# Kernel optimization log

Hardware: AMD Instinct MI355X
Metric: run time of the kernel (lower is better)

## Reference

```python
import jax, jax.numpy as jnp
import numpy as np

N = 4096   # total atoms in batch
G = 32     # graphs in batch
T = 4      # number of atom types


def setup_inputs() -> dict:
    key = jax.random.key(0)
    ks = jax.random.split(key, 12)
    types = jax.random.randint(ks[0], (N,), 0, T)
    node_attrs = jax.nn.one_hot(types, T, dtype=jnp.float32)
    batch = jnp.repeat(jnp.arange(G, dtype=jnp.int32), N // G)  # sorted graph ids
    # interatomic distances, kept away from 0 to avoid 1/R**6 blowup
    R = jax.random.uniform(ks[1], (N, N), minval=0.5, maxval=5.0, dtype=jnp.float32)
    R = 0.5 * (R + R.T)
    F_cut = jax.random.uniform(ks[2], (N, N), dtype=jnp.float32)
    ref_A = jax.random.uniform(ks[3], (T, T), dtype=jnp.float32)
    ref_B = jax.random.uniform(ks[4], (T, T), dtype=jnp.float32)
    ref_C = jax.random.uniform(ks[5], (T, T), dtype=jnp.float32)
    ref_D = jax.random.uniform(ks[6], (T, T), dtype=jnp.float32)
    ref_mu = jax.random.uniform(ks[7], (T, T), dtype=jnp.float32)
    electric_energy = jax.random.normal(ks[8], (G, 1), dtype=jnp.float32)
    atomic_electric_energy = jax.random.normal(ks[9], (N, 1), dtype=jnp.float32)
    short_energy = jax.random.normal(ks[10], (G, 1), dtype=jnp.float32)
    atomic_short_energy = jax.random.normal(ks[11], (N, 1), dtype=jnp.float32)
    return dict(node_attrs=node_attrs, R=R, F_cut=F_cut,
                ref_A=ref_A, ref_B=ref_B, ref_C=ref_C, ref_D=ref_D, ref_mu=ref_mu,
                electric_energy=electric_energy,
                atomic_electric_energy=atomic_electric_energy,
                short_energy=short_energy, atomic_short_energy=atomic_short_energy,
                batch=batch)


def reference(node_attrs, R, F_cut, ref_A, ref_B, ref_C, ref_D, ref_mu,
              electric_energy, atomic_electric_energy,
              short_energy, atomic_short_energy, batch):
    n = node_attrs.shape[0]
    types = jnp.argmax(node_attrs, axis=1)                 # [N] atom type ids
    ti, tj = types[:, None], types[None, :]
    # intra-graph (block-diagonal) mask replaces the per-graph Python loop
    same = (batch[:, None] == batch[None, :]).astype(R.dtype)  # [N,N]
    A = ref_A[ti, tj]
    B = ref_B[ti, tj]
    C = ref_C[ti, tj]
    D = ref_D[ti, tj]
    mu = ref_mu[ti, tj]
    R6 = R ** 6
    # Buckingham-like pair potential; zero off-block and on the diagonal
    E_2b_ij = (A * jnp.exp(B * (mu - R)) - C / R6 - D / (R6 * R * R)) * F_cut * same
    E_2b_ij = jnp.where(jnp.eye(n, dtype=bool), jnp.zeros((), E_2b_ij.dtype), E_2b_ij)
    atomic_E_2b = (jnp.sum(E_2b_ij, axis=-1) * 0.5)[:, None]   # [N,1]
    E_2b = jax.ops.segment_sum(atomic_E_2b, batch, num_segments=G)  # [G,1]
    energy = electric_energy + E_2b + short_energy                   # [G,1]
    node_energy = atomic_electric_energy + atomic_E_2b + atomic_short_energy  # [N,1]
    return energy, node_energy
```

## Files before the change

kernel.cpp:

```cpp
#include <hip/hip_runtime.h>


template <int GSZ, int BPG>
__global__ __launch_bounds__(256) void te_part_kernel(
    const float* __restrict__ node_attrs,
    const float* __restrict__ Rm,
    const float* __restrict__ Fm,
    const float* __restrict__ rA,
    const float* __restrict__ rB,
    const float* __restrict__ rC,
    const float* __restrict__ rD,
    const float* __restrict__ rMu,
    const float* __restrict__ aelec,
    const float* __restrict__ ashort,
    const int* __restrict__ batch,
    float* __restrict__ out,
    float* __restrict__ ws,
    int n, int g) {
  constexpr int RPB = GSZ / BPG;
  constexpr int WAVES = 4;
  constexpr int RPW = RPB / WAVES;
  constexpr int CPL = GSZ / 64;

  const int b = blockIdx.x / BPG;
  const int c = blockIdx.x % BPG;
  const int gbase = b * GSZ;

  __shared__ float tab[5 * 16];
  __shared__ int   stype[GSZ];
  __shared__ int   sbatch[GSZ];
  __shared__ float wpart[WAVES];

  const int t = threadIdx.x;
  const int wave = t >> 6;
  const int lane = t & 63;
  const int row0 = c * RPB + wave * RPW;

  float rv[RPW][CPL], fv[RPW][CPL];
#pragma unroll
  for (int r = 0; r < RPW; ++r) {
    const size_t off = (size_t)(gbase + row0 + r) * n + gbase;
#pragma unroll
    for (int q = 0; q < CPL; ++q) {
      rv[r][q] = Rm[off + lane + q * 64];
      fv[r][q] = Fm[off + lane + q * 64];
    }
  }

  if (t < 16) {
    tab[t]      = rA[t];
    tab[16 + t] = rB[t];
    tab[32 + t] = rC[t];
    tab[48 + t] = rD[t];
    tab[64 + t] = rMu[t];
  }
  if (t < GSZ) {
    const float4 v = *(const float4*)(node_attrs + (size_t)(gbase + t) * 4);
    int bt = 0;
    float best = v.x;
    if (v.y > best) { best = v.y; bt = 1; }
    if (v.z > best) { best = v.z; bt = 2; }
    if (v.w > best) { best = v.w; bt = 3; }
    stype[t]  = bt;
    sbatch[t] = batch[gbase + t];
  }
  __syncthreads();

  float bpart = 0.f;
#pragma unroll
  for (int r = 0; r < RPW; ++r) {
    const int rl  = row0 + r;
    const int bi  = sbatch[rl];
    const int ti4 = stype[rl] * 4;
    float acc = 0.f;
#pragma unroll
    for (int q = 0; q < CPL; ++q) {
      const int jl = lane + q * 64;
      if (sbatch[jl] == bi && jl != rl) {
        float rr = rv[r][q];
        float f  = fv[r][q];
        int idx = ti4 + stype[jl];
        float r2 = rr * rr;
        float r6 = r2 * r2 * r2;
        float val = tab[idx] * __expf(tab[16 + idx] * (tab[64 + idx] - rr))
                    - tab[32 + idx] / r6
                    - tab[48 + idx] / (r6 * r2);
        acc += val * f;
      }
    }
#pragma unroll
    for (int o = 32; o > 0; o >>= 1) acc += __shfl_down(acc, o, 64);
    if (lane == 0) {
      const int gi = gbase + rl;
      float half = 0.5f * acc;
      out[g + gi] = aelec[gi] + half + ashort[gi];
      bpart += half;
    }
  }
  if (lane == 0) wpart[wave] = bpart;
  __syncthreads();

  if (t == 0) {
    float s = 0.f;
#pragma unroll
    for (int w = 0; w < WAVES; ++w) s += wpart[w];
    ws[blockIdx.x] = s;
  }
}

__global__ __launch_bounds__(64) void te_finish_kernel(
    const float* __restrict__ electric,
    const float* __restrict__ shorte,
    const float* __restrict__ ws,
    float* __restrict__ out,
    int g, int bpg) {
  int t = threadIdx.x;
  if (t < g) {
    float s = 0.f;
    for (int c = 0; c < bpg; ++c) s += ws[t * bpg + c];
    out[t] = electric[t] + s + shorte[t];
  }
}

__global__ __launch_bounds__(1024) void te_group_kernel(
    const float* __restrict__ node_attrs,
    const float* __restrict__ Rm,
    const float* __restrict__ Fm,
    const float* __restrict__ rA,
    const float* __restrict__ rB,
    const float* __restrict__ rC,
    const float* __restrict__ rD,
    const float* __restrict__ rMu,
    const float* __restrict__ electric,
    const float* __restrict__ aelec,
    const float* __restrict__ shorte,
    const float* __restrict__ ashort,
    const int* __restrict__ batch,
    float* __restrict__ out,
    int n, int g) {
  const int gsz = n / g;
  const int gbase = blockIdx.x * gsz;

  __shared__ float tab[5 * 16];
  __shared__ int   stype[128];
  __shared__ int   sbatch[128];
  __shared__ float snode[128];
  __shared__ float wsum[16];

  int t = threadIdx.x;
  if (t < 16) {
    tab[t]      = rA[t];
    tab[16 + t] = rB[t];
    tab[32 + t] = rC[t];
    tab[48 + t] = rD[t];
    tab[64 + t] = rMu[t];
  }
  if (t < gsz) {
    const float4 v = *(const float4*)(node_attrs + (size_t)(gbase + t) * 4);
    int bt = 0;
    float best = v.x;
    if (v.y > best) { best = v.y; bt = 1; }
    if (v.z > best) { best = v.z; bt = 2; }
    if (v.w > best) { best = v.w; bt = 3; }
    stype[t]  = bt;
    sbatch[t] = batch[gbase + t];
    snode[t]  = aelec[gbase + t] + ashort[gbase + t];
  }
  __syncthreads();

  const int wave = t >> 6;
  const int lane = t & 63;
  const int rpw = (gsz + 15) >> 4;
  const int r0 = wave * rpw;
  const int r1 = (r0 + rpw < gsz) ? (r0 + rpw) : gsz;

  float gpart = 0.f;
  for (int rl = r0; rl < r1; ++rl) {
    const int gi  = gbase + rl;
    const int bi  = sbatch[rl];
    const int ti4 = stype[rl] * 4;
    const float* Rrow = Rm + (size_t)gi * n + gbase;
    const float* Frow = Fm + (size_t)gi * n + gbase;

    float acc = 0.f;
    for (int jl = lane; jl < gsz; jl += 64) {
      if (sbatch[jl] == bi && jl != rl) {
        float r = Rrow[jl];
        float f = Frow[jl];
        int idx = ti4 + stype[jl];
        float r2 = r * r;
        float r6 = r2 * r2 * r2;
        float val = tab[idx] * __expf(tab[16 + idx] * (tab[64 + idx] - r))
                    - tab[32 + idx] / r6
                    - tab[48 + idx] / (r6 * r2);
        acc += val * f;
      }
    }
#pragma unroll
    for (int o = 32; o > 0; o >>= 1) acc += __shfl_down(acc, o, 64);
    if (lane == 0) {
      float half = 0.5f * acc;
      out[g + gi] = snode[rl] + half;
      gpart += half;
    }
  }
  if (lane == 0) wsum[wave] = (r0 < gsz) ? gpart : 0.f;
  __syncthreads();

  if (t == 0) {
    float s = 0.f;
#pragma unroll
    for (int w = 0; w < 16; ++w) s += wsum[w];
    int b = sbatch[0];
    out[b] = electric[b] + s + shorte[b];
  }
}

extern "C" void kernel_launch(void* const* d_in, const int* in_sizes, int n_in,
                              void* d_out, int out_size, void* d_ws, size_t ws_size,
                              hipStream_t stream) {
  const float* node_attrs = (const float*)d_in[0];
  const float* Rm         = (const float*)d_in[1];
  const float* Fm         = (const float*)d_in[2];
  const float* rA         = (const float*)d_in[3];
  const float* rB         = (const float*)d_in[4];
  const float* rC         = (const float*)d_in[5];
  const float* rD         = (const float*)d_in[6];
  const float* rMu        = (const float*)d_in[7];
  const float* electric   = (const float*)d_in[8];
  const float* aelec      = (const float*)d_in[9];
  const float* shorte     = (const float*)d_in[10];
  const float* ashort     = (const float*)d_in[11];
  const int*   batch      = (const int*)d_in[12];

  int n = in_sizes[12];
  int g = in_sizes[8];
  float* out = (float*)d_out;
  float* ws  = (float*)d_ws;

  if (n / g == 128 && n % g == 0) {
    constexpr int BPG = 8;
    te_part_kernel<128, BPG><<<g * BPG, 256, 0, stream>>>(
        node_attrs, Rm, Fm, rA, rB, rC, rD, rMu, aelec, ashort, batch,
        out, ws, n, g);
    te_finish_kernel<<<1, 64, 0, stream>>>(electric, shorte, ws, out, g, BPG);
  } else {
    te_group_kernel<<<g, 1024, 0, stream>>>(node_attrs, Rm, Fm, rA, rB, rC, rD,
                                            rMu, electric, aelec, shorte,
                                            ashort, batch, out, n, g);
  }
}
```

Measured before the change: 12.62 us.

## Fuse per-graph partial sums and finish kernel into one block per graph

Replaces the two-kernel scheme (8 blocks of 256 threads per graph writing partials, then a finish kernel) with one 1024-thread block per graph. That block computes every row of its graph's diagonal block and writes the graph energy directly. This removes the second launch and the workspace round trip. In exchange there are only 32 blocks, which leaves most compute units idle during the memory-bound load of the R and F blocks.

```diff
diff --git a/kernel.cpp b/kernel.cpp
--- a/kernel.cpp
+++ b/kernel.cpp
@@ -1,8 +1,8 @@
 #include <hip/hip_runtime.h>
 
 
-template <int GSZ, int BPG>
-__global__ __launch_bounds__(256) void te_part_kernel(
+template <int GSZ>
+__global__ __launch_bounds__(1024, 4) void te_fused_kernel(
     const float* __restrict__ node_attrs,
     const float* __restrict__ Rm,
     const float* __restrict__ Fm,
@@ -11,39 +11,42 @@
     const float* __restrict__ rC,
     const float* __restrict__ rD,
     const float* __restrict__ rMu,
+    const float* __restrict__ electric,
     const float* __restrict__ aelec,
+    const float* __restrict__ shorte,
     const float* __restrict__ ashort,
     const int* __restrict__ batch,
     float* __restrict__ out,
-    float* __restrict__ ws,
     int n, int g) {
-  constexpr int RPB = GSZ / BPG;
-  constexpr int WAVES = 4;
-  constexpr int RPW = RPB / WAVES;
+  constexpr int WAVES = 16;
+  constexpr int RPW = GSZ / WAVES;
   constexpr int CPL = GSZ / 64;
 
-  const int b = blockIdx.x / BPG;
-  const int c = blockIdx.x % BPG;
+  const int b = blockIdx.x;
   const int gbase = b * GSZ;
 
   __shared__ float tab[5 * 16];
   __shared__ int   stype[GSZ];
   __shared__ int   sbatch[GSZ];
-  __shared__ float wpart[WAVES];
+  __shared__ float snode[GSZ];
+  __shared__ float wsum[WAVES];
 
   const int t = threadIdx.x;
   const int wave = t >> 6;
   const int lane = t & 63;
-  const int row0 = c * RPB + wave * RPW;
+  const int row0 = wave * RPW;
+
+  const float eb = electric[b];
+  const float sb = shorte[b];
 
   float rv[RPW][CPL], fv[RPW][CPL];
 #pragma unroll
   for (int r = 0; r < RPW; ++r) {
-    const size_t off = (size_t)(gbase + row0 + r) * n + gbase;
+    const size_t off = (size_t)(gbase + row0 + r) * n + gbase + lane;
 #pragma unroll
     for (int q = 0; q < CPL; ++q) {
-      rv[r][q] = Rm[off + lane + q * 64];
-      fv[r][q] = Fm[off + lane + q * 64];
+      rv[r][q] = Rm[off + q * 64];
+      fv[r][q] = Fm[off + q * 64];
     }
   }
 
@@ -63,10 +66,11 @@
     if (v.w > best) { best = v.w; bt = 3; }
     stype[t]  = bt;
     sbatch[t] = batch[gbase + t];
-  }
-  __syncthreads();
-
-  float bpart = 0.f;
+    snode[t]  = aelec[gbase + t] + ashort[gbase + t];
+  }
+  __syncthreads();
+
+  float gpart = 0.f;
 #pragma unroll
   for (int r = 0; r < RPW; ++r) {
     const int rl  = row0 + r;
@@ -93,32 +97,18 @@
     if (lane == 0) {
       const int gi = gbase + rl;
       float half = 0.5f * acc;
-      out[g + gi] = aelec[gi] + half + ashort[gi];
-      bpart += half;
-    }
-  }
-  if (lane == 0) wpart[wave] = bpart;
+      out[g + gi] = snode[rl] + half;
+      gpart += half;
+    }
+  }
+  if (lane == 0) wsum[wave] = gpart;
   __syncthreads();
 
   if (t == 0) {
     float s = 0.f;
 #pragma unroll
-    for (int w = 0; w < WAVES; ++w) s += wpart[w];
-    ws[blockIdx.x] = s;
-  }
-}
-
-__global__ __launch_bounds__(64) void te_finish_kernel(
-    const float* __restrict__ electric,
-    const float* __restrict__ shorte,
-    const float* __restrict__ ws,
-    float* __restrict__ out,
-    int g, int bpg) {
-  int t = threadIdx.x;
-  if (t < g) {
-    float s = 0.f;
-    for (int c = 0; c < bpg; ++c) s += ws[t * bpg + c];
-    out[t] = electric[t] + s + shorte[t];
+    for (int w = 0; w < WAVES; ++w) s += wsum[w];
+    out[b] = eb + s + sb;
   }
 }
 
@@ -211,8 +201,8 @@
     float s = 0.f;
 #pragma unroll
     for (int w = 0; w < 16; ++w) s += wsum[w];
-    int b = sbatch[0];
-    out[b] = electric[b] + s + shorte[b];
+    int bb = sbatch[0];
+    out[bb] = electric[bb] + s + shorte[bb];
   }
 }
 
@@ -236,14 +226,11 @@
   int n = in_sizes[12];
   int g = in_sizes[8];
   float* out = (float*)d_out;
-  float* ws  = (float*)d_ws;
-
-  if (n / g == 128 && n % g == 0) {
-    constexpr int BPG = 8;
-    te_part_kernel<128, BPG><<<g * BPG, 256, 0, stream>>>(
-        node_attrs, Rm, Fm, rA, rB, rC, rD, rMu, aelec, ashort, batch,
-        out, ws, n, g);
-    te_finish_kernel<<<1, 64, 0, stream>>>(electric, shorte, ws, out, g, BPG);
+
+  if (g > 0 && n % g == 0 && n / g == 128) {
+    te_fused_kernel<128><<<g, 1024, 0, stream>>>(
+        node_attrs, Rm, Fm, rA, rB, rC, rD, rMu, electric, aelec, shorte,
+        ashort, batch, out, n, g);
   } else {
     te_group_kernel<<<g, 1024, 0, stream>>>(node_attrs, Rm, Fm, rA, rB, rC, rD,
                                             rMu, electric, aelec, shorte,
```

New measurement: 13.26 us. +5.1%, slower.
